# Optimization experiments

Measured on AMD Instinct MI355X. Metric: run time of the kernel, lower is better.

The kernel has to match this reference:

```python
import jax, jax.numpy as jnp
import numpy as np

N_NODES = 100000
N_EDGES = 3200000
D_FEAT = 512
D_HID = 64
D_LAT = 16
N_CLASS = 10
N_FLOW = 10
K_PROP = 10
ALPHA_TELEPORT = 0.1


def setup_inputs() -> dict:
    key = jax.random.key(0)
    ks = jax.random.split(key, 8)
    x = jax.random.normal(ks[0], (N_NODES, D_FEAT), jnp.float32)
    edge_index = jax.random.randint(ks[1], (2, N_EDGES), 0, N_NODES)
    p_c = jax.random.uniform(ks[2], (N_CLASS,), jnp.float32) + 0.1
    p_c = p_c / p_c.sum()
    W1 = jax.random.normal(ks[3], (D_FEAT, D_HID), jnp.float32) / np.sqrt(D_FEAT).astype(np.float32)
    b1 = jnp.zeros((D_HID,), jnp.float32)
    W2 = jax.random.normal(ks[4], (D_HID, D_LAT), jnp.float32) / np.sqrt(D_HID).astype(np.float32)
    b2 = jnp.zeros((D_LAT,), jnp.float32)
    flow_z0 = jax.random.normal(ks[5], (N_FLOW, N_CLASS, D_LAT), jnp.float32) * 0.1
    flow_alpha_prime = jax.random.normal(ks[6], (N_FLOW, N_CLASS, 1), jnp.float32) * 0.1
    flow_beta = jax.random.normal(ks[7], (N_FLOW, N_CLASS, 1), jnp.float32) * 0.1
    return dict(x=x, edge_index=edge_index, p_c=p_c, W1=W1, b1=b1, W2=W2, b2=b2,
                flow_z0=flow_z0, flow_alpha_prime=flow_alpha_prime, flow_beta=flow_beta)


def _batched_radial_log_prob(z, flow_z0, flow_alpha_prime, flow_beta):
    # Per-class batched radial flow (invertible pyro-style parameterization).
    # z: [N, D] -> log_q: [N, C]
    C, D = flow_z0.shape[1], flow_z0.shape[2]
    zz = jnp.broadcast_to(z[None], (C, z.shape[0], D))  # [C, N, D]
    sum_logdet = jnp.zeros((C, z.shape[0]), z.dtype)
    for l in range(flow_z0.shape[0]):  # small fixed number of flow layers
        z0 = flow_z0[l][:, None, :]                               # [C,1,D]
        alpha = jax.nn.softplus(flow_alpha_prime[l])[:, None, :]  # [C,1,1]
        beta_hat = -alpha + jax.nn.softplus(flow_beta[l])[:, None, :]
        dz = zz - z0
        r = jnp.sqrt(jnp.sum(dz * dz, axis=-1, keepdims=True))    # [C,N,1]
        h = 1.0 / (alpha + r)
        bh = beta_hat * h
        zz = zz + bh * dz
        logdet = (D - 1) * jnp.log1p(bh) + jnp.log1p(bh - beta_hat * r * h * h)
        sum_logdet = sum_logdet + logdet[..., 0]
    log_base = -0.5 * jnp.sum(zz * zz, axis=-1) - 0.5 * D * jnp.log(2.0 * jnp.pi)
    return (log_base + sum_logdet).T  # [N, C]


def _appnp(beta_ft, edge_index, n_nodes):
    # APPNP with self loops and symmetric gcn normalization over edge list.
    src = jnp.concatenate([edge_index[0], jnp.arange(n_nodes)])
    dst = jnp.concatenate([edge_index[1], jnp.arange(n_nodes)])
    deg = jax.ops.segment_sum(jnp.ones_like(src, dtype=beta_ft.dtype), dst, num_segments=n_nodes)
    dinv = jnp.where(deg > 0, jax.lax.rsqrt(jnp.maximum(deg, 1.0)), 0.0)
    norm = (dinv[src] * dinv[dst])[:, None]  # [E+N, 1]
    x0 = beta_ft
    b = beta_ft
    for _ in range(K_PROP):
        agg = jax.ops.segment_sum(norm * b[src], dst, num_segments=n_nodes)
        b = (1.0 - ALPHA_TELEPORT) * agg + ALPHA_TELEPORT * x0
    return b


def reference(x, edge_index, p_c, W1, b1, W2, b2, flow_z0, flow_alpha_prime, flow_beta):
    h = jax.nn.relu(x @ W1 + b1)           # input_encoder (dropout inactive at eval)
    z = h @ W2 + b2                        # latent_encoder, [N, D_LAT]
    log_q = _batched_radial_log_prob(z, flow_z0, flow_alpha_prime, flow_beta)
    log_q_per_class = log_q + jnp.log(p_c)[None, :]
    log_scale = 0.5 * D_LAT * jnp.log(4.0 * jnp.pi)  # 'latent-new' evidence scale
    beta_ft = jnp.exp(jnp.clip(log_q_per_class + log_scale, -30.0, 30.0))
    beta = _appnp(beta_ft, edge_index, x.shape[0])
    alpha = 1.0 + beta
    soft = alpha / jnp.sum(alpha, axis=-1, keepdims=True)
    hard = jnp.argmax(soft, axis=-1)
    return hard[:, None], soft
```

## Files before the change

kernel.cpp:

```cpp
#include <hip/hip_runtime.h>
#include <math.h>
#include <limits.h>

#define DF 512
#define DH 64
#define DL 16
#define NC 10
#define NF 10
#define KPROP 10

#define BSH 7
#define BW  (1 << BSH)
#define MAXB 1024
#define TILE 16384
#define TS 16384

__device__ __forceinline__ float softplus_(float x){
  return fmaxf(x, 0.0f) + log1pf(expf(-fabsf(x)));
}

#define BM 128
#define BK2 16
__global__ __launch_bounds__(256) void k_gemm1z(const float* __restrict__ x,
    const float* __restrict__ W1, const float* __restrict__ b1,
    const float* __restrict__ W2, const float* __restrict__ b2,
    float* __restrict__ z, int N)
{
  __shared__ float At[BK2][132];
  __shared__ float Bs[BK2][68];
  __shared__ float W2s[DH][20];
  __shared__ float b2s[DL];
  const int tid = threadIdx.x;
  for (int i = tid; i < DH*DL; i += 256) W2s[i>>4][i&15] = W2[i];
  if (tid < DL) b2s[tid] = b2[tid];
  const int tx = tid & 15, ty = tid >> 4;
  const int row0 = blockIdx.x * BM;
  float acc[8][4] = {};
  for (int k0 = 0; k0 < DF; k0 += BK2){
    #pragma unroll
    for (int j = 0; j < 2; ++j){
      int s_ = tid + j*256;
      int r  = s_ >> 2;
      int k4 = (s_ & 3) << 2;
      int row = row0 + r;
      float4 va = make_float4(0.f,0.f,0.f,0.f);
      if (row < N) va = *(const float4*)&x[(size_t)row*DF + k0 + k4];
      At[k4+0][r]=va.x; At[k4+1][r]=va.y; At[k4+2][r]=va.z; At[k4+3][r]=va.w;
    }
    {
      int kk = tid >> 4, c4 = (tid & 15) << 2;
      float4 vb = *(const float4*)&W1[(size_t)(k0+kk)*DH + c4];
      *(float4*)&Bs[kk][c4] = vb;
    }
    __syncthreads();
    #pragma unroll
    for (int kk = 0; kk < BK2; ++kk){
      float4 a0 = *(const float4*)&At[kk][ty*8];
      float4 a1 = *(const float4*)&At[kk][ty*8+4];
      float4 bv = *(const float4*)&Bs[kk][tx*4];
      float a8[8] = {a0.x,a0.y,a0.z,a0.w,a1.x,a1.y,a1.z,a1.w};
      float b4[4] = {bv.x,bv.y,bv.z,bv.w};
      #pragma unroll
      for (int i=0;i<8;++i)
        #pragma unroll
        for (int j=0;j<4;++j) acc[i][j] = fmaf(a8[i], b4[j], acc[i][j]);
    }
    __syncthreads();
  }
  float4 bias = ((const float4*)b1)[tx];
  float bb[4] = {bias.x, bias.y, bias.z, bias.w};
  #pragma unroll
  for (int i=0;i<8;++i)
    #pragma unroll
    for (int j=0;j<4;++j) acc[i][j] = fmaxf(acc[i][j] + bb[j], 0.0f);

  #pragma unroll 1
  for (int r = 0; r < 8; ++r){
    float zp[16];
    #pragma unroll
    for (int zc=0; zc<16; ++zc) zp[zc] = 0.f;
    #pragma unroll
    for (int j=0; j<4; ++j){
      int c = tx*4 + j;
      float h = acc[r][j];
      float4 w0 = *(const float4*)&W2s[c][0];
      float4 w1 = *(const float4*)&W2s[c][4];
      float4 w2 = *(const float4*)&W2s[c][8];
      float4 w3 = *(const float4*)&W2s[c][12];
      zp[0]=fmaf(h,w0.x,zp[0]);  zp[1]=fmaf(h,w0.y,zp[1]);
      zp[2]=fmaf(h,w0.z,zp[2]);  zp[3]=fmaf(h,w0.w,zp[3]);
      zp[4]=fmaf(h,w1.x,zp[4]);  zp[5]=fmaf(h,w1.y,zp[5]);
      zp[6]=fmaf(h,w1.z,zp[6]);  zp[7]=fmaf(h,w1.w,zp[7]);
      zp[8]=fmaf(h,w2.x,zp[8]);  zp[9]=fmaf(h,w2.y,zp[9]);
      zp[10]=fmaf(h,w2.z,zp[10]); zp[11]=fmaf(h,w2.w,zp[11]);
      zp[12]=fmaf(h,w3.x,zp[12]); zp[13]=fmaf(h,w3.y,zp[13]);
      zp[14]=fmaf(h,w3.z,zp[14]); zp[15]=fmaf(h,w3.w,zp[15]);
    }
    #pragma unroll
    for (int zc=0; zc<16; ++zc){
      float v = zp[zc];
      v += __shfl_xor(v, 1, 16);
      v += __shfl_xor(v, 2, 16);
      v += __shfl_xor(v, 4, 16);
      v += __shfl_xor(v, 8, 16);
      zp[zc] = v;
    }
    int grow = row0 + ty*8 + r;
    if (tx < 4 && grow < N){
      float4 o;
      if      (tx == 0) o = make_float4(zp[0]+b2s[0],  zp[1]+b2s[1],  zp[2]+b2s[2],  zp[3]+b2s[3]);
      else if (tx == 1) o = make_float4(zp[4]+b2s[4],  zp[5]+b2s[5],  zp[6]+b2s[6],  zp[7]+b2s[7]);
      else if (tx == 2) o = make_float4(zp[8]+b2s[8],  zp[9]+b2s[9],  zp[10]+b2s[10],zp[11]+b2s[11]);
      else              o = make_float4(zp[12]+b2s[12],zp[13]+b2s[13],zp[14]+b2s[14],zp[15]+b2s[15]);
      ((float4*)z)[(size_t)grow*4 + tx] = o;
    }
  }
}

__global__ __launch_bounds__(256) void k_flow2(const float* __restrict__ z,
    const float* __restrict__ pc, const float* __restrict__ z0g,
    const float* __restrict__ apg, const float* __restrict__ fbg,
    const float* __restrict__ dinv,
    float* __restrict__ x0, float* __restrict__ c0, float* __restrict__ y0, int N)
{
  __shared__ float z0s[NF][NC][DL];
  __shared__ float alps[NF][NC];
  __shared__ float bhs[NF][NC];
  __shared__ float lpc[NC];
  int tid = threadIdx.x;
  for (int i = tid; i < NF*NC*DL; i += 256)
    z0s[(i>>4)/NC][(i>>4)%NC][i&15] = z0g[i];
  if (tid < NF*NC){
    int l = tid/NC, c = tid%NC;
    float al = softplus_(apg[tid]);
    alps[l][c] = al;
    bhs[l][c]  = -al + softplus_(fbg[tid]);
  }
  if (tid < NC) lpc[tid] = __logf(pc[tid]);
  __syncthreads();

  int idx = blockIdx.x*256 + tid;
  int n = idx >> 4, c = idx & 15;
  if (n >= N) return;
  float dn = dinv[n];
  if (c >= NC){ x0[idx] = 0.f; c0[idx] = 0.f; y0[idx] = 0.f; return; }

  float zz[DL];
  const float4* z4 = (const float4*)z;
  #pragma unroll
  for (int q=0; q<4; ++q){
    float4 v = z4[(size_t)n*4 + q];
    zz[q*4+0]=v.x; zz[q*4+1]=v.y; zz[q*4+2]=v.z; zz[q*4+3]=v.w;
  }
  const float NEGHALFD_LOG2PI = -14.703016531274762f;
  const float LOGSCALE        =  20.248193975754326f;
  float sld = 0.f;
  #pragma unroll 1
  for (int l=0; l<NF; ++l){
    float al = alps[l][c], bhat = bhs[l][c];
    float dz[DL]; float r2 = 0.f;
    #pragma unroll
    for (int d=0; d<DL; ++d){ float t = zz[d] - z0s[l][c][d]; dz[d]=t; r2 = fmaf(t,t,r2); }
    float r  = sqrtf(r2);
    float hh = 1.0f/(al + r);
    float bh = bhat*hh;
    #pragma unroll
    for (int d=0; d<DL; ++d) zz[d] = fmaf(bh, dz[d], zz[d]);
    sld += 15.0f*__logf(1.0f + bh) + __logf(1.0f + bh - bhat*r*hh*hh);
  }
  float q2 = 0.f;
  #pragma unroll
  for (int d=0; d<DL; ++d) q2 = fmaf(zz[d], zz[d], q2);
  float v = -0.5f*q2 + NEGHALFD_LOG2PI + sld + lpc[c] + LOGSCALE;
  v = fminf(fmaxf(v, -30.f), 30.f);
  float xv = __expf(v);
  x0[idx] = xv;
  c0[idx] = dn*xv;
  y0[idx] = 0.1f*dn*xv;
}

__global__ __launch_bounds__(256) void k_bhist(const int* __restrict__ dst,
    int* __restrict__ bCnt, int E, int B)
{
  __shared__ int hh[MAXB];
  int tid = threadIdx.x;
  for (int b = tid; b < B; b += 256) hh[b] = 0;
  __syncthreads();
  for (int i = blockIdx.x*256 + tid; i < E; i += gridDim.x*256)
    atomicAdd(&hh[dst[i] >> BSH], 1);
  __syncthreads();
  for (int b = tid; b < B; b += 256) if (hh[b]) atomicAdd(&bCnt[b], hh[b]);
}

__global__ void k_bscan(const int* __restrict__ bCnt, int* __restrict__ bOff, int B){
  if (blockIdx.x==0 && threadIdx.x==0){
    int run = 0;
    for (int b=0;b<B;++b){ bOff[b]=run; run+=bCnt[b]; }
    bOff[B]=run;
  }
}

__global__ __launch_bounds__(256) void k_bscatter(const int* __restrict__ src,
    const int* __restrict__ dst, const int* __restrict__ bOff,
    int* __restrict__ bCur, int* __restrict__ bp, int E, int B)
{
  __shared__ int hc[MAXB];
  __shared__ int hb[MAXB];
  int tid = threadIdx.x;
  int base = blockIdx.x * TILE;
  int lim  = base + TILE; if (lim > E) lim = E;
  for (int b = tid; b < B; b += 256) hc[b] = 0;
  __syncthreads();
  for (int i = base + tid; i < lim; i += 256)
    atomicAdd(&hc[dst[i] >> BSH], 1);
  __syncthreads();
  for (int b = tid; b < B; b += 256){
    int c = hc[b];
    hb[b] = c ? atomicAdd(&bCur[b], c) : 0;
    hc[b] = 0;
  }
  __syncthreads();
  for (int i = base + tid; i < lim; i += 256){
    int d = dst[i];
    int b = d >> BSH;
    int pos = bOff[b] + hb[b] + atomicAdd(&hc[b], 1);
    bp[pos] = (src[i] << BSH) | (d & (BW-1));
  }
}

__global__ __launch_bounds__(256) void k_bdeg(const int* __restrict__ bp,
    const int* __restrict__ bOff, int* __restrict__ deg,
    float* __restrict__ dinv, float* __restrict__ dinv2, int N)
{
  __shared__ int cur[BW];
  int tid = threadIdx.x;
  int b = blockIdx.x;
  if (tid < BW) cur[tid] = 0;
  __syncthreads();
  int s = bOff[b], e = bOff[b+1];
  for (int i = s + tid; i < e; i += 256)
    atomicAdd(&cur[bp[i] & (BW-1)], 1);
  __syncthreads();
  int node = (b << BSH) + tid;
  if (tid < BW && node < N){
    int d = cur[tid] + 1;
    deg[node] = d;
    float dv = 1.0f / sqrtf((float)d);
    dinv[node]  = dv;
    dinv2[node] = dv*dv;
  }
}

__global__ __launch_bounds__(256) void k_scan_part(const int* __restrict__ deg,
    int* __restrict__ part, int N){
  __shared__ int sd[256];
  int base = blockIdx.x*1024;
  int tid = threadIdx.x;
  int s = 0;
  #pragma unroll
  for (int i=0;i<4;++i){ int idx = base + tid*4 + i; if (idx < N) s += deg[idx]; }
  sd[tid] = s; __syncthreads();
  for (int ofs=128; ofs>0; ofs>>=1){ if (tid<ofs) sd[tid]+=sd[tid+ofs]; __syncthreads(); }
  if (tid==0) part[blockIdx.x] = sd[0];
}

__global__ void k_scan_top(int* part, int nb){
  if (blockIdx.x==0 && threadIdx.x==0){
    int run = 0;
    for (int i=0;i<nb;++i){ int v = part[i]; part[i] = run; run += v; }
  }
}

__global__ __launch_bounds__(256) void k_scan_final(const int* __restrict__ deg,
    const int* __restrict__ part, int* __restrict__ off, int N, int E)
{
  __shared__ int sc[256];
  int base = blockIdx.x*1024;
  int tid = threadIdx.x;
  int v[4]; int s = 0;
  #pragma unroll
  for (int i=0;i<4;++i){ int idx = base + tid*4 + i; v[i] = (idx<N)?deg[idx]:0; s += v[i]; }
  sc[tid] = s; __syncthreads();
  for (int ofs=1; ofs<256; ofs<<=1){
    int t = (tid>=ofs) ? sc[tid-ofs] : 0;
    __syncthreads();
    sc[tid] += t;
    __syncthreads();
  }
  int ex = sc[tid] - s + part[blockIdx.x];
  #pragma unroll
  for (int i=0;i<4;++i){
    int idx = base + tid*4 + i;
    if (idx < N){
      off[idx] = ex;
      if (idx == N-1) off[N] = ex + v[i];
      ex += v[i];
    }
  }
}

__global__ __launch_bounds__(256) void k_place(const int* __restrict__ bp,
    const int* __restrict__ bOff, const int* __restrict__ off,
    int* __restrict__ csr, int N)
{
  __shared__ int cur[BW];
  int tid = threadIdx.x;
  int b = blockIdx.x;
  int node0 = b << BSH;
  if (tid < BW){
    cur[tid] = 1;
    int node = node0 + tid;
    if (node < N) csr[off[node]] = node;
  }
  __syncthreads();
  int s = bOff[b], e = bOff[b+1];
  for (int i = s + tid; i < e; i += 256){
    int v  = bp[i];
    int dl = v & (BW-1);
    int sn = v >> BSH;
    int d  = node0 + dl;
    int p  = off[d] + atomicAdd(&cur[dl], 1);
    csr[p] = sn;
  }
}

__global__ __launch_bounds__(256) void k_rank(int* __restrict__ csr,
    const int* __restrict__ off, unsigned short* __restrict__ tb, int N)
{
  int wid  = (blockIdx.x*256 + threadIdx.x) >> 6;
  int lane = threadIdx.x & 63;
  if (wid >= N) return;
  int s = off[wid], e = off[wid+1];
  int d = e - s;
  if (d <= 0){
    if (lane < 8) tb[(size_t)wid*8 + lane] = 0;
    return;
  }
  if (d <= 64){
    int v = (lane < d) ? csr[s+lane] : INT_MAX;
    int rank = 0;
    for (int j = 0; j < d; ++j){
      int bv = __shfl(v, j);
      rank += (bv < v) || (bv == v && j < lane);
    }
    if (lane < d) csr[s+rank] = v;
    unsigned int myc = (unsigned)d;
    #pragma unroll
    for (int t = 0; t < 7; ++t){
      unsigned long long m = __ballot((lane < d) && (v < (t+1)*TS));
      if (lane == t) myc = (unsigned)__popcll(m);
    }
    if (lane < 8) tb[(size_t)wid*8 + lane] = (unsigned short)((lane < 7) ? myc : (unsigned)d);
  } else if (d <= 256){
    int v0 = (lane      < d) ? csr[s+lane      ] : INT_MAX;
    int v1 = (lane+64   < d) ? csr[s+lane+64   ] : INT_MAX;
    int v2 = (lane+128  < d) ? csr[s+lane+128  ] : INT_MAX;
    int v3 = (lane+192  < d) ? csr[s+lane+192  ] : INT_MAX;
    int r0=0,r1=0,r2=0,r3=0;
    for (int j = 0; j < d; ++j){
      int slot = j >> 6, jl = j & 63;
      int bv = (slot==0) ? __shfl(v0,jl) : (slot==1) ? __shfl(v1,jl)
             : (slot==2) ? __shfl(v2,jl) : __shfl(v3,jl);
      r0 += (bv < v0) || (bv == v0 && j < lane);
      r1 += (bv < v1) || (bv == v1 && j < lane+64);
      r2 += (bv < v2) || (bv == v2 && j < lane+128);
      r3 += (bv < v3) || (bv == v3 && j < lane+192);
    }
    if (lane      < d) csr[s+r0]=v0;
    if (lane+64   < d) csr[s+r1]=v1;
    if (lane+128  < d) csr[s+r2]=v2;
    if (lane+192  < d) csr[s+r3]=v3;
    unsigned int myc = (unsigned)d;
    #pragma unroll
    for (int t = 0; t < 7; ++t){
      int lim = (t+1)*TS;
      unsigned long long m0 = __ballot((lane      < d) && (v0 < lim));
      unsigned long long m1 = __ballot((lane+64   < d) && (v1 < lim));
      unsigned long long m2 = __ballot((lane+128  < d) && (v2 < lim));
      unsigned long long m3 = __ballot((lane+192  < d) && (v3 < lim));
      if (lane == t)
        myc = (unsigned)(__popcll(m0)+__popcll(m1)+__popcll(m2)+__popcll(m3));
    }
    if (lane < 8) tb[(size_t)wid*8 + lane] = (unsigned short)((lane < 7) ? myc : (unsigned)d);
  } else {
    if (lane == 0){
      for (int i = s+1; i < e; ++i){
        int key = csr[i]; int j = i-1;
        while (j >= s && csr[j] > key){ csr[j+1] = csr[j]; --j; }
        csr[j+1] = key;
      }
      for (int t = 0; t < 7; ++t){
        int lim = (t+1)*TS;
        int c = 0;
        for (int i = s; i < e; ++i) c += (csr[i] < lim);
        tb[(size_t)wid*8 + t] = (unsigned short)c;
      }
      tb[(size_t)wid*8 + 7] = (unsigned short)d;
    }
  }
}

__global__ __launch_bounds__(256) void k_prop(const float* __restrict__ cin,
    const float* __restrict__ y0, const float* __restrict__ dinv2,
    float* __restrict__ cout, const int* __restrict__ csr,
    const int* __restrict__ off, const unsigned short* __restrict__ tb,
    int N, int NT)
{
  int t0 = blockIdx.x*256 + threadIdx.x;
  int n = t0 >> 2, q = t0 & 3;
  bool valid = (n < N);
  int nc = valid ? n : (N-1);
  const float4* c4 = (const float4*)cin;
  float4 a = make_float4(0.f,0.f,0.f,0.f);
  int s = off[nc], e = off[nc+1];
  uint4 bw = *(const uint4*)(tb + (size_t)nc*8);
  if (!valid) e = s;
  int i = s;
  #pragma unroll
  for (int t = 0; t < 8; ++t){
    if (t < NT){
      int lim;
      if (t == NT-1) lim = e;
      else {
        unsigned w = (t < 2) ? bw.x : (t < 4) ? bw.y : (t < 6) ? bw.z : bw.w;
        unsigned c = (t & 1) ? (w >> 16) : (w & 0xffffu);
        lim = s + (int)c;
        if (lim > e) lim = e;
      }
      for (; i+4 <= lim; i += 4){
        int s0=csr[i], s1=csr[i+1], s2=csr[i+2], s3=csr[i+3];
        float4 v0 = c4[(size_t)s0*4 + q];
        float4 v1 = c4[(size_t)s1*4 + q];
        float4 v2 = c4[(size_t)s2*4 + q];
        float4 v3 = c4[(size_t)s3*4 + q];
        a.x+=v0.x; a.y+=v0.y; a.z+=v0.z; a.w+=v0.w;
        a.x+=v1.x; a.y+=v1.y; a.z+=v1.z; a.w+=v1.w;
        a.x+=v2.x; a.y+=v2.y; a.z+=v2.z; a.w+=v2.w;
        a.x+=v3.x; a.y+=v3.y; a.z+=v3.z; a.w+=v3.w;
      }
      for (; i < lim; ++i){
        float4 v = c4[(size_t)csr[i]*4 + q];
        a.x+=v.x; a.y+=v.y; a.z+=v.z; a.w+=v.w;
      }
      __syncthreads();
    }
  }
  if (valid){
    float w9 = 0.9f * dinv2[n];
    float4 yv = ((const float4*)y0)[(size_t)n*4 + q];
    float4 o;
    o.x = fmaf(w9, a.x, yv.x);
    o.y = fmaf(w9, a.y, yv.y);
    o.z = fmaf(w9, a.z, yv.z);
    o.w = fmaf(w9, a.w, yv.w);
    ((float4*)cout)[(size_t)n*4 + q] = o;
  }
}

__global__ __launch_bounds__(256) void k_prop_final(const float* __restrict__ cin,
    const float* __restrict__ x0, const float* __restrict__ dinv,
    const int* __restrict__ csr, const int* __restrict__ off,
    const unsigned short* __restrict__ tb,
    float* __restrict__ out, int N, int NT)
{
  int t0 = blockIdx.x*256 + threadIdx.x;
  int n = t0 >> 2, q = t0 & 3;
  bool valid = (n < N);
  int nc = valid ? n : (N-1);
  const float4* c4 = (const float4*)cin;
  float4 a = make_float4(0.f,0.f,0.f,0.f);
  int s = off[nc], e = off[nc+1];
  uint4 bw = *(const uint4*)(tb + (size_t)nc*8);
  if (!valid) e = s;
  int i = s;
  #pragma unroll
  for (int t = 0; t < 8; ++t){
    if (t < NT){
      int lim;
      if (t == NT-1) lim = e;
      else {
        unsigned w = (t < 2) ? bw.x : (t < 4) ? bw.y : (t < 6) ? bw.z : bw.w;
        unsigned c = (t & 1) ? (w >> 16) : (w & 0xffffu);
        lim = s + (int)c;
        if (lim > e) lim = e;
      }
      for (; i+4 <= lim; i += 4){
        int s0=csr[i], s1=csr[i+1], s2=csr[i+2], s3=csr[i+3];
        float4 v0 = c4[(size_t)s0*4 + q];
        float4 v1 = c4[(size_t)s1*4 + q];
        float4 v2 = c4[(size_t)s2*4 + q];
        float4 v3 = c4[(size_t)s3*4 + q];
        a.x+=v0.x; a.y+=v0.y; a.z+=v0.z; a.w+=v0.w;
        a.x+=v1.x; a.y+=v1.y; a.z+=v1.z; a.w+=v1.w;
        a.x+=v2.x; a.y+=v2.y; a.z+=v2.z; a.w+=v2.w;
        a.x+=v3.x; a.y+=v3.y; a.z+=v3.z; a.w+=v3.w;
      }
      for (; i < lim; ++i){
        float4 v = c4[(size_t)csr[i]*4 + q];
        a.x+=v.x; a.y+=v.y; a.z+=v.z; a.w+=v.w;
      }
      __syncthreads();
    }
  }
  if (!valid) return;
  float w9 = 0.9f * dinv[n];
  float4 xv = ((const float4*)x0)[(size_t)n*4 + q];
  float4 al;
  al.x = fmaf(w9, a.x, fmaf(0.1f, xv.x, 1.f));
  al.y = fmaf(w9, a.y, fmaf(0.1f, xv.y, 1.f));
  al.z = fmaf(w9, a.z, fmaf(0.1f, xv.z, 1.f));
  al.w = fmaf(w9, a.w, fmaf(0.1f, xv.w, 1.f));

  float sv = 0.f;
  if (q < 2)       sv = al.x + al.y + al.z + al.w;
  else if (q == 2) sv = al.x + al.y;
  sv += __shfl_xor(sv, 1, 4);
  sv += __shfl_xor(sv, 2, 4);

  float bv = -1e30f; int bi = 999;
  int cb = q*4;
  int nvalid = (q < 2) ? 4 : (q == 2 ? 2 : 0);
  float av[4] = {al.x, al.y, al.z, al.w};
  for (int j = 0; j < nvalid; ++j){
    if (av[j] > bv){ bv = av[j]; bi = cb + j; }
  }
  #pragma unroll
  for (int o = 1; o <= 2; o <<= 1){
    float vo = __shfl_xor(bv, o, 4);
    int  io  = __shfl_xor(bi, o, 4);
    if (vo > bv || (vo == bv && io < bi)){ bv = vo; bi = io; }
  }

  float inv = 1.0f / sv;
  size_t sb = (size_t)N + (size_t)n*NC;
  for (int j = 0; j < nvalid; ++j) out[sb + cb + j] = av[j] * inv;
  if (q == 0) out[n] = (float)bi;
}

extern "C" void kernel_launch(void* const* d_in, const int* in_sizes, int n_in,
                              void* d_out, int out_size, void* d_ws, size_t ws_size,
                              hipStream_t stream)
{
  const float* x  = (const float*)d_in[0];
  const int*   ei = (const int*)  d_in[1];
  const float* pc = (const float*)d_in[2];
  const float* W1 = (const float*)d_in[3];
  const float* b1 = (const float*)d_in[4];
  const float* W2 = (const float*)d_in[5];
  const float* b2 = (const float*)d_in[6];
  const float* z0 = (const float*)d_in[7];
  const float* ap = (const float*)d_in[8];
  const float* fb = (const float*)d_in[9];
  float* out = (float*)d_out;

  const int N = in_sizes[0] / DF;
  const int E = in_sizes[1] / 2;
  const int* src = ei;
  const int* dst = ei + E;
  const int B = (N + BW - 1) >> BSH;
  const int NT = (N + TS - 1) / TS;

  char* ws = (char*)d_ws;
  size_t o = 0;
  size_t region0 = (size_t)E*sizeof(int);
  if ((size_t)N*DL*sizeof(float) > region0) region0 = (size_t)N*DL*sizeof(float);
  int*   bp   = (int*)  (ws + o);
  float* z    = (float*)(ws + o);
  o += region0;
  int*   csr  = (int*)  (ws + o); o += (size_t)(E+N)*sizeof(int);
  float* x0   = (float*)(ws + o); o += (size_t)N*DL*sizeof(float);
  float* c0   = (float*)(ws + o); o += (size_t)N*DL*sizeof(float);
  float* y0   = (float*)(ws + o); o += (size_t)N*DL*sizeof(float);
  float* cA   = (float*)(ws + o); o += (size_t)N*DL*sizeof(float);
  float* cB   = (float*)(ws + o); o += (size_t)N*DL*sizeof(float);
  int*   deg  = (int*)  (ws + o); o += (size_t)N*sizeof(int);
  float* dinv = (float*)(ws + o); o += (size_t)N*sizeof(float);
  float* dinv2= (float*)(ws + o); o += (size_t)N*sizeof(float);
  unsigned short* tb = (unsigned short*)(ws + o); o += (size_t)N*8*sizeof(unsigned short);
  int*   offs = (int*)  (ws + o); o += (size_t)(N+2)*sizeof(int);
  int*   part = (int*)  (ws + o); o += 4096;
  int*   bCnt = (int*)  (ws + o); o += MAXB*sizeof(int);
  int*   bOff = (int*)  (ws + o); o += (MAXB+1)*sizeof(int);
  int*   bCur = (int*)  (ws + o); o += MAXB*sizeof(int);

  const int TB = 256;
  int nb  = (N + 1023) / 1024;

  hipMemsetAsync(bCnt, 0, MAXB*sizeof(int), stream);
  hipMemsetAsync(bCur, 0, MAXB*sizeof(int), stream);
  k_bhist<<<512, TB, 0, stream>>>(dst, bCnt, E, B);
  k_bscan<<<1, 1, 0, stream>>>(bCnt, bOff, B);
  k_bscatter<<<(E + TILE - 1)/TILE, TB, 0, stream>>>(src, dst, bOff, bCur, bp, E, B);
  k_bdeg<<<B, TB, 0, stream>>>(bp, bOff, deg, dinv, dinv2, N);
  k_scan_part<<<nb, TB, 0, stream>>>(deg, part, N);
  k_scan_top<<<1, 1, 0, stream>>>(part, nb);
  k_scan_final<<<nb, TB, 0, stream>>>(deg, part, offs, N, E);
  k_place<<<B, TB, 0, stream>>>(bp, bOff, offs, csr, N);
  k_rank<<<(N + 3) / 4, TB, 0, stream>>>(csr, offs, tb, N);

  k_gemm1z<<<(N + BM - 1) / BM, TB, 0, stream>>>(x, W1, b1, W2, b2, z, N);
  k_flow2<<<((N*DL) + TB - 1) / TB, TB, 0, stream>>>(z, pc, z0, ap, fb, dinv,
                                                     x0, c0, y0, N);

  int gP = ((N*4) + TB - 1) / TB;
  const float* cin = c0;
  for (int it = 0; it < KPROP-1; ++it){
    float* cout = (it & 1) ? cB : cA;
    k_prop<<<gP, TB, 0, stream>>>(cin, y0, dinv2, cout, csr, offs, tb, N, NT);
    cin = cout;
  }
  k_prop_final<<<gP, TB, 0, stream>>>(cin, x0, dinv, csr, offs, tb, out, N, NT);
}
```

Measured before the change: 807.2 us.

## Retile fused GEMM with shared-memory second layer; unroll propagation gathers by eight

The fused x@W1→relu→@W2 kernel moves from 128-row/16-k tiles to 64-row/32-k tiles. The hidden activations are now staged in shared memory so the second small GEMM runs as a direct per-row dot product, replacing the 16-way shuffle reduction. The propagation kernels unroll the neighbour gather to eight independent loads and split the sums across two accumulators to expose more memory-level parallelism. The cost is a smaller GEMM tile with less register reuse per thread, and a changed floating-point summation order.

New measurement: 785.2 us. 2.7% less time.

```diff
diff --git a/kernel.cpp b/kernel.cpp
--- a/kernel.cpp
+++ b/kernel.cpp
@@ -19,102 +19,77 @@
   return fmaxf(x, 0.0f) + log1pf(expf(-fabsf(x)));
 }
 
-#define BM 128
-#define BK2 16
+#define BM 64
+#define BN 64
+#define BK 32
 __global__ __launch_bounds__(256) void k_gemm1z(const float* __restrict__ x,
     const float* __restrict__ W1, const float* __restrict__ b1,
     const float* __restrict__ W2, const float* __restrict__ b2,
     float* __restrict__ z, int N)
 {
-  __shared__ float At[BK2][132];
-  __shared__ float Bs[BK2][68];
-  __shared__ float W2s[DH][20];
+  __shared__ float smem[2*BK*(BM+4)];
+  float (*At)[BM+4] = (float(*)[BM+4])smem;
+  float (*Bs)[BN+4] = (float(*)[BN+4])(smem + BK*(BM+4));
+  __shared__ float W2s[DH][DL];
   __shared__ float b2s[DL];
   const int tid = threadIdx.x;
   for (int i = tid; i < DH*DL; i += 256) W2s[i>>4][i&15] = W2[i];
   if (tid < DL) b2s[tid] = b2[tid];
   const int tx = tid & 15, ty = tid >> 4;
   const int row0 = blockIdx.x * BM;
-  float acc[8][4] = {};
-  for (int k0 = 0; k0 < DF; k0 += BK2){
+  float acc[4][4] = {};
+  for (int k0 = 0; k0 < DF; k0 += BK) {
     #pragma unroll
-    for (int j = 0; j < 2; ++j){
-      int s_ = tid + j*256;
-      int r  = s_ >> 2;
-      int k4 = (s_ & 3) << 2;
+    for (int i = 0; i < 2; ++i) {
+      int idx = tid + i*256;
+      int r  = idx >> 3;
+      int kk = (idx & 7) << 2;
       int row = row0 + r;
       float4 va = make_float4(0.f,0.f,0.f,0.f);
-      if (row < N) va = *(const float4*)&x[(size_t)row*DF + k0 + k4];
-      At[k4+0][r]=va.x; At[k4+1][r]=va.y; At[k4+2][r]=va.z; At[k4+3][r]=va.w;
-    }
-    {
-      int kk = tid >> 4, c4 = (tid & 15) << 2;
-      float4 vb = *(const float4*)&W1[(size_t)(k0+kk)*DH + c4];
-      *(float4*)&Bs[kk][c4] = vb;
+      if (row < N) va = *(const float4*)&x[(size_t)row*DF + k0 + kk];
+      At[kk+0][r]=va.x; At[kk+1][r]=va.y; At[kk+2][r]=va.z; At[kk+3][r]=va.w;
+      int r2 = idx >> 4;
+      int c4 = (idx & 15) << 2;
+      float4 vb = *(const float4*)&W1[(size_t)(k0+r2)*DH + c4];
+      Bs[r2][c4+0]=vb.x; Bs[r2][c4+1]=vb.y; Bs[r2][c4+2]=vb.z; Bs[r2][c4+3]=vb.w;
     }
     __syncthreads();
     #pragma unroll
-    for (int kk = 0; kk < BK2; ++kk){
-      float4 a0 = *(const float4*)&At[kk][ty*8];
-      float4 a1 = *(const float4*)&At[kk][ty*8+4];
-      float4 bv = *(const float4*)&Bs[kk][tx*4];
-      float a8[8] = {a0.x,a0.y,a0.z,a0.w,a1.x,a1.y,a1.z,a1.w};
-      float b4[4] = {bv.x,bv.y,bv.z,bv.w};
+    for (int kk = 0; kk < BK; ++kk) {
+      float4 av = *(const float4*)&At[kk][ty<<2];
+      float4 bv = *(const float4*)&Bs[kk][tx<<2];
+      float a4[4]={av.x,av.y,av.z,av.w};
+      float b4[4]={bv.x,bv.y,bv.z,bv.w};
       #pragma unroll
-      for (int i=0;i<8;++i)
+      for (int i=0;i<4;++i)
         #pragma unroll
-        for (int j=0;j<4;++j) acc[i][j] = fmaf(a8[i], b4[j], acc[i][j]);
+        for (int j=0;j<4;++j) acc[i][j] = fmaf(a4[i], b4[j], acc[i][j]);
     }
     __syncthreads();
   }
   float4 bias = ((const float4*)b1)[tx];
-  float bb[4] = {bias.x, bias.y, bias.z, bias.w};
-  #pragma unroll
-  for (int i=0;i<8;++i)
+  float bias4[4] = {bias.x, bias.y, bias.z, bias.w};
+  float (*hs)[BM+4] = (float(*)[BM+4])smem;
+  #pragma unroll
+  for (int i=0;i<4;++i){
     #pragma unroll
-    for (int j=0;j<4;++j) acc[i][j] = fmaxf(acc[i][j] + bb[j], 0.0f);
-
-  #pragma unroll 1
-  for (int r = 0; r < 8; ++r){
-    float zp[16];
-    #pragma unroll
-    for (int zc=0; zc<16; ++zc) zp[zc] = 0.f;
-    #pragma unroll
-    for (int j=0; j<4; ++j){
-      int c = tx*4 + j;
-      float h = acc[r][j];
-      float4 w0 = *(const float4*)&W2s[c][0];
-      float4 w1 = *(const float4*)&W2s[c][4];
-      float4 w2 = *(const float4*)&W2s[c][8];
-      float4 w3 = *(const float4*)&W2s[c][12];
-      zp[0]=fmaf(h,w0.x,zp[0]);  zp[1]=fmaf(h,w0.y,zp[1]);
-      zp[2]=fmaf(h,w0.z,zp[2]);  zp[3]=fmaf(h,w0.w,zp[3]);
-      zp[4]=fmaf(h,w1.x,zp[4]);  zp[5]=fmaf(h,w1.y,zp[5]);
-      zp[6]=fmaf(h,w1.z,zp[6]);  zp[7]=fmaf(h,w1.w,zp[7]);
-      zp[8]=fmaf(h,w2.x,zp[8]);  zp[9]=fmaf(h,w2.y,zp[9]);
-      zp[10]=fmaf(h,w2.z,zp[10]); zp[11]=fmaf(h,w2.w,zp[11]);
-      zp[12]=fmaf(h,w3.x,zp[12]); zp[13]=fmaf(h,w3.y,zp[13]);
-      zp[14]=fmaf(h,w3.z,zp[14]); zp[15]=fmaf(h,w3.w,zp[15]);
-    }
-    #pragma unroll
-    for (int zc=0; zc<16; ++zc){
-      float v = zp[zc];
-      v += __shfl_xor(v, 1, 16);
-      v += __shfl_xor(v, 2, 16);
-      v += __shfl_xor(v, 4, 16);
-      v += __shfl_xor(v, 8, 16);
-      zp[zc] = v;
-    }
-    int grow = row0 + ty*8 + r;
-    if (tx < 4 && grow < N){
-      float4 o;
-      if      (tx == 0) o = make_float4(zp[0]+b2s[0],  zp[1]+b2s[1],  zp[2]+b2s[2],  zp[3]+b2s[3]);
-      else if (tx == 1) o = make_float4(zp[4]+b2s[4],  zp[5]+b2s[5],  zp[6]+b2s[6],  zp[7]+b2s[7]);
-      else if (tx == 2) o = make_float4(zp[8]+b2s[8],  zp[9]+b2s[9],  zp[10]+b2s[10],zp[11]+b2s[11]);
-      else              o = make_float4(zp[12]+b2s[12],zp[13]+b2s[13],zp[14]+b2s[14],zp[15]+b2s[15]);
-      ((float4*)z)[(size_t)grow*4 + tx] = o;
-    }
-  }
+    for (int j=0;j<4;++j)
+      hs[(ty<<2)+i][(tx<<2)+j] = fmaxf(acc[i][j] + bias4[j], 0.0f);
+  }
+  __syncthreads();
+  int row = tid >> 2, lg = tid & 3;
+  float4 zacc = ((const float4*)b2s)[lg];
+  #pragma unroll 8
+  for (int k = 0; k < DH; ++k){
+    float hv = hs[row][k];
+    float4 wv = *(const float4*)&W2s[k][lg<<2];
+    zacc.x = fmaf(hv, wv.x, zacc.x);
+    zacc.y = fmaf(hv, wv.y, zacc.y);
+    zacc.z = fmaf(hv, wv.z, zacc.z);
+    zacc.w = fmaf(hv, wv.w, zacc.w);
+  }
+  int grow = row0 + row;
+  if (grow < N) ((float4*)z)[(size_t)grow*4 + lg] = zacc;
 }
 
 __global__ __launch_bounds__(256) void k_flow2(const float* __restrict__ z,
@@ -411,7 +386,8 @@
   bool valid = (n < N);
   int nc = valid ? n : (N-1);
   const float4* c4 = (const float4*)cin;
-  float4 a = make_float4(0.f,0.f,0.f,0.f);
+  float4 a0 = make_float4(0.f,0.f,0.f,0.f);
+  float4 a1 = make_float4(0.f,0.f,0.f,0.f);
   int s = off[nc], e = off[nc+1];
   uint4 bw = *(const uint4*)(tb + (size_t)nc*8);
   if (!valid) e = s;
@@ -427,20 +403,37 @@
         lim = s + (int)c;
         if (lim > e) lim = e;
       }
-      for (; i+4 <= lim; i += 4){
-        int s0=csr[i], s1=csr[i+1], s2=csr[i+2], s3=csr[i+3];
+      for (; i+8 <= lim; i += 8){
+        int s0=csr[i],   s1=csr[i+1], s2=csr[i+2], s3=csr[i+3];
+        int s4=csr[i+4], s5=csr[i+5], s6=csr[i+6], s7=csr[i+7];
         float4 v0 = c4[(size_t)s0*4 + q];
         float4 v1 = c4[(size_t)s1*4 + q];
         float4 v2 = c4[(size_t)s2*4 + q];
         float4 v3 = c4[(size_t)s3*4 + q];
-        a.x+=v0.x; a.y+=v0.y; a.z+=v0.z; a.w+=v0.w;
-        a.x+=v1.x; a.y+=v1.y; a.z+=v1.z; a.w+=v1.w;
-        a.x+=v2.x; a.y+=v2.y; a.z+=v2.z; a.w+=v2.w;
-        a.x+=v3.x; a.y+=v3.y; a.z+=v3.z; a.w+=v3.w;
-      }
-      for (; i < lim; ++i){
+        float4 v4 = c4[(size_t)s4*4 + q];
+        float4 v5 = c4[(size_t)s5*4 + q];
+        float4 v6 = c4[(size_t)s6*4 + q];
+        float4 v7 = c4[(size_t)s7*4 + q];
+        a0.x+=v0.x; a0.y+=v0.y; a0.z+=v0.z; a0.w+=v0.w;
+        a1.x+=v1.x; a1.y+=v1.y; a1.z+=v1.z; a1.w+=v1.w;
+        a0.x+=v2.x; a0.y+=v2.y; a0.z+=v2.z; a0.w+=v2.w;
+        a1.x+=v3.x; a1.y+=v3.y; a1.z+=v3.z; a1.w+=v3.w;
+        a0.x+=v4.x; a0.y+=v4.y; a0.z+=v4.z; a0.w+=v4.w;
+        a1.x+=v5.x; a1.y+=v5.y; a1.z+=v5.z; a1.w+=v5.w;
+        a0.x+=v6.x; a0.y+=v6.y; a0.z+=v6.z; a0.w+=v6.w;
+        a1.x+=v7.x; a1.y+=v7.y; a1.z+=v7.z; a1.w+=v7.w;
+      }
+      for (; i+2 <= lim; i += 2){
+        int s0=csr[i], s1=csr[i+1];
+        float4 v0 = c4[(size_t)s0*4 + q];
+        float4 v1 = c4[(size_t)s1*4 + q];
+        a0.x+=v0.x; a0.y+=v0.y; a0.z+=v0.z; a0.w+=v0.w;
+        a1.x+=v1.x; a1.y+=v1.y; a1.z+=v1.z; a1.w+=v1.w;
+      }
+      if (i < lim){
         float4 v = c4[(size_t)csr[i]*4 + q];
-        a.x+=v.x; a.y+=v.y; a.z+=v.z; a.w+=v.w;
+        a0.x+=v.x; a0.y+=v.y; a0.z+=v.z; a0.w+=v.w;
+        ++i;
       }
       __syncthreads();
     }
@@ -449,10 +442,10 @@
     float w9 = 0.9f * dinv2[n];
     float4 yv = ((const float4*)y0)[(size_t)n*4 + q];
     float4 o;
-    o.x = fmaf(w9, a.x, yv.x);
-    o.y = fmaf(w9, a.y, yv.y);
-    o.z = fmaf(w9, a.z, yv.z);
-    o.w = fmaf(w9, a.w, yv.w);
+    o.x = fmaf(w9, a0.x+a1.x, yv.x);
+    o.y = fmaf(w9, a0.y+a1.y, yv.y);
+    o.z = fmaf(w9, a0.z+a1.z, yv.z);
+    o.w = fmaf(w9, a0.w+a1.w, yv.w);
     ((float4*)cout)[(size_t)n*4 + q] = o;
   }
 }
@@ -468,7 +461,8 @@
   bool valid = (n < N);
   int nc = valid ? n : (N-1);
   const float4* c4 = (const float4*)cin;
-  float4 a = make_float4(0.f,0.f,0.f,0.f);
+  float4 a0 = make_float4(0.f,0.f,0.f,0.f);
+  float4 a1 = make_float4(0.f,0.f,0.f,0.f);
   int s = off[nc], e = off[nc+1];
   uint4 bw = *(const uint4*)(tb + (size_t)nc*8);
   if (!valid) e = s;
@@ -484,20 +478,37 @@
         lim = s + (int)c;
         if (lim > e) lim = e;
       }
-      for (; i+4 <= lim; i += 4){
-        int s0=csr[i], s1=csr[i+1], s2=csr[i+2], s3=csr[i+3];
+      for (; i+8 <= lim; i += 8){
+        int s0=csr[i],   s1=csr[i+1], s2=csr[i+2], s3=csr[i+3];
+        int s4=csr[i+4], s5=csr[i+5], s6=csr[i+6], s7=csr[i+7];
         float4 v0 = c4[(size_t)s0*4 + q];
         float4 v1 = c4[(size_t)s1*4 + q];
         float4 v2 = c4[(size_t)s2*4 + q];
         float4 v3 = c4[(size_t)s3*4 + q];
-        a.x+=v0.x; a.y+=v0.y; a.z+=v0.z; a.w+=v0.w;
-        a.x+=v1.x; a.y+=v1.y; a.z+=v1.z; a.w+=v1.w;
-        a.x+=v2.x; a.y+=v2.y; a.z+=v2.z; a.w+=v2.w;
-        a.x+=v3.x; a.y+=v3.y; a.z+=v3.z; a.w+=v3.w;
-      }
-      for (; i < lim; ++i){
+        float4 v4 = c4[(size_t)s4*4 + q];
+        float4 v5 = c4[(size_t)s5*4 + q];
+        float4 v6 = c4[(size_t)s6*4 + q];
+        float4 v7 = c4[(size_t)s7*4 + q];
+        a0.x+=v0.x; a0.y+=v0.y; a0.z+=v0.z; a0.w+=v0.w;
+        a1.x+=v1.x; a1.y+=v1.y; a1.z+=v1.z; a1.w+=v1.w;
+        a0.x+=v2.x; a0.y+=v2.y; a0.z+=v2.z; a0.w+=v2.w;
+        a1.x+=v3.x; a1.y+=v3.y; a1.z+=v3.z; a1.w+=v3.w;
+        a0.x+=v4.x; a0.y+=v4.y; a0.z+=v4.z; a0.w+=v4.w;
+        a1.x+=v5.x; a1.y+=v5.y; a1.z+=v5.z; a1.w+=v5.w;
+        a0.x+=v6.x; a0.y+=v6.y; a0.z+=v6.z; a0.w+=v6.w;
+        a1.x+=v7.x; a1.y+=v7.y; a1.z+=v7.z; a1.w+=v7.w;
+      }
+      for (; i+2 <= lim; i += 2){
+        int s0=csr[i], s1=csr[i+1];
+        float4 v0 = c4[(size_t)s0*4 + q];
+        float4 v1 = c4[(size_t)s1*4 + q];
+        a0.x+=v0.x; a0.y+=v0.y; a0.z+=v0.z; a0.w+=v0.w;
+        a1.x+=v1.x; a1.y+=v1.y; a1.z+=v1.z; a1.w+=v1.w;
+      }
+      if (i < lim){
         float4 v = c4[(size_t)csr[i]*4 + q];
-        a.x+=v.x; a.y+=v.y; a.z+=v.z; a.w+=v.w;
+        a0.x+=v.x; a0.y+=v.y; a0.z+=v.z; a0.w+=v.w;
+        ++i;
       }
       __syncthreads();
     }
@@ -506,10 +517,10 @@
   float w9 = 0.9f * dinv[n];
   float4 xv = ((const float4*)x0)[(size_t)n*4 + q];
   float4 al;
-  al.x = fmaf(w9, a.x, fmaf(0.1f, xv.x, 1.f));
-  al.y = fmaf(w9, a.y, fmaf(0.1f, xv.y, 1.f));
-  al.z = fmaf(w9, a.z, fmaf(0.1f, xv.z, 1.f));
-  al.w = fmaf(w9, a.w, fmaf(0.1f, xv.w, 1.f));
+  al.x = fmaf(w9, a0.x+a1.x, fmaf(0.1f, xv.x, 1.f));
+  al.y = fmaf(w9, a0.y+a1.y, fmaf(0.1f, xv.y, 1.f));
+  al.z = fmaf(w9, a0.z+a1.z, fmaf(0.1f, xv.z, 1.f));
+  al.w = fmaf(w9, a0.w+a1.w, fmaf(0.1f, xv.w, 1.f));
 
   float sv = 0.f;
   if (q < 2)       sv = al.x + al.y + al.z + al.w;
```
